# Kernel optimization log

Hardware: AMD Instinct MI355X
Metric: run time of the kernel (lower is better)

Reference implementation:

```python
import jax, jax.numpy as jnp
import numpy as np

B, N, F = 2, 512, 64
LN_EPS = 1e-6

def _ln(x, scale, bias):
    mu = jnp.mean(x, axis=-1, keepdims=True)
    var = jnp.mean(jnp.square(x - mu), axis=-1, keepdims=True)
    return (x - mu) * jax.lax.rsqrt(var + LN_EPS) * scale + bias

def setup_inputs() -> dict:
    key = jax.random.key(0)
    k = jax.random.split(key, 16)
    w = lambda kk, s: jax.random.normal(kk, s, jnp.float32) * 0.02
    return {
        'qs': jax.random.normal(k[0], (B, N, F), jnp.float32),
        'ks': jax.random.normal(k[1], (B, N, F), jnp.float32),
        'vs': jax.random.normal(k[2], (B, N, F), jnp.float32),
        'qs_s': jax.random.normal(k[3], (B, N, 2), jnp.float32),
        'ks_s': jax.random.normal(k[4], (B, N, 2), jnp.float32),
        'qs_t': jax.random.uniform(k[5], (B, N, 1), dtype=jnp.float32),
        'ks_t': jax.random.uniform(k[6], (B, N, 1), dtype=jnp.float32),
        'valid_lens': jax.random.randint(k[7], (B,), 1, N + 1),
        'Wv': w(k[8], (F, 64)), 'bv': jnp.zeros((64,), jnp.float32),
        'Wa1': w(k[9], (2 * F + 5, 256)), 'ba1': jnp.zeros((256,), jnp.float32),
        'Wa2': w(k[10], (256, 256)), 'ba2': jnp.zeros((256,), jnp.float32),
        'Wa3': w(k[11], (256, 1)), 'ba3': jnp.zeros((1,), jnp.float32),
        'Wg1': w(k[12], (64, 256)), 'bg1': jnp.zeros((256,), jnp.float32),
        'Wg2': w(k[13], (256, 64)), 'bg2': jnp.zeros((64,), jnp.float32),
        'ln1_s': jnp.ones((64,), jnp.float32), 'ln1_b': jnp.zeros((64,), jnp.float32),
        'ln2_s': jnp.ones((64,), jnp.float32), 'ln2_b': jnp.zeros((64,), jnp.float32),
    }

def reference(qs, ks, vs, qs_s, ks_s, qs_t, ks_t, valid_lens,
              Wv, bv, Wa1, ba1, Wa2, ba2, Wa3, ba3,
              Wg1, bg1, Wg2, bg2, ln1_s, ln1_b, ln2_s, ln2_b):
    Bb, Q, Ff = qs.shape
    K = ks.shape[1]
    # pairwise broadcast-concat features: (B, Q, K, 2F+5)
    qb = jnp.broadcast_to(qs[:, :, None, :], (Bb, Q, K, Ff))
    kb = jnp.broadcast_to(ks[:, None, :, :], (Bb, Q, K, Ff))
    s_diff = qs_s[:, :, None, :] - ks_s[:, None, :, :]            # (B,Q,K,2)
    s_dist = jnp.linalg.norm(s_diff, axis=-1, keepdims=True)      # (B,Q,K,1)
    t_diff = qs_t[:, :, None, :] - ks_t[:, None, :, :]            # (B,Q,K,1)
    m = jnp.concatenate([qb, kb, s_diff, s_dist, jnp.square(s_dist), t_diff], axis=-1)
    # validity mask over the node axis (Q == K node-set attention)
    v_mask = (jnp.arange(K)[None, :] < valid_lens[:, None])[..., None]  # (B,K,1)
    mask = jnp.logical_and(v_mask, t_diff[..., 0] > 0)                   # (B,Q,K)
    # per-pair MLP attention score
    h = jax.nn.gelu(m @ Wa1 + ba1)
    h = jax.nn.gelu(h @ Wa2 + ba2)
    attn = (h @ Wa3 + ba3)[..., 0]                                       # (B,Q,K)
    attn = jnp.where(mask, attn, 0.0)
    vproj = vs @ Wv + bv                                                 # (B,K,64)
    ctx = _ln(jnp.einsum('bqk,bkd->bqd', attn, vproj), ln1_s, ln1_b)     # (B,Q,64)
    gate = jax.nn.gelu(ctx @ Wg1 + bg1) @ Wg2 + bg2                      # (B,Q,64)
    pooled = jnp.max(jnp.where(v_mask, gate * ctx, -jnp.inf), axis=1)    # (B,64)
    vnode = _ln(pooled, ln2_s, ln2_b)
    return ctx, vnode
```

## Files before the change

kernel.cpp:

```cpp
#include <hip/hip_runtime.h>
#include <math.h>

#define BB 2
#define NN 512
#define FF 64
#define HH 256
#define LN_EPS 1e-6f

typedef __attribute__((ext_vector_type(8))) short short8v;
typedef __attribute__((ext_vector_type(4))) float float4v;

#define LDAH 264

#if __has_builtin(__builtin_amdgcn_exp2f)
#define EXP2F(x) __builtin_amdgcn_exp2f(x)
#else
#define EXP2F(x) exp2f(x)
#endif
#if __has_builtin(__builtin_amdgcn_sqrtf)
#define SQRTF(x) __builtin_amdgcn_sqrtf(x)
#else
#define SQRTF(x) sqrtf(x)
#endif

__device__ __forceinline__ float gelu_tanh(float x) {
    float x2 = x * x;
    float t  = __builtin_fmaf(0.10294340f, x2, 2.30211830f);
    float e  = EXP2F(x * t);
    float r  = __builtin_amdgcn_rcpf(e + 1.0f);
    return __builtin_fmaf(-x, r, x);
}

__device__ __forceinline__ unsigned short f2bf(float f) {
    unsigned u = __float_as_uint(f);
    unsigned r = u + 0x7fffu + ((u >> 16) & 1u);
    return (unsigned short)(r >> 16);
}

__device__ __forceinline__ unsigned enc_f(float f) {
    unsigned b = __float_as_uint(f);
    return (b & 0x80000000u) ? ~b : (b | 0x80000000u);
}
__device__ __forceinline__ float dec_f(unsigned u) {
    return __uint_as_float((u & 0x80000000u) ? (u ^ 0x80000000u) : ~u);
}

__global__ __launch_bounds__(256) void prep_kernel(
    const float* __restrict__ qs, const float* __restrict__ ks,
    const float* __restrict__ vs,
    const float* __restrict__ Wa1, const float* __restrict__ ba1,
    const float* __restrict__ Wv,  const float* __restrict__ bv,
    const float* __restrict__ Wa2,
    const float* __restrict__ qs_t, const float* __restrict__ ks_t,
    const int*   __restrict__ valid_lens,
    const float* __restrict__ ln1_b,
    float* __restrict__ Aq, float* __restrict__ Ak,
    float* __restrict__ vproj, unsigned short* __restrict__ Wa2T,
    int* __restrict__ klist, int* __restrict__ wl,
    unsigned* __restrict__ pooled,
    float* __restrict__ ctx_init) {
    __shared__ int s_cnt[8];
    __shared__ int s_off[9];
    const int bid = blockIdx.x;
    const int t   = threadIdx.x;
    if (bid < 1024) {
        int idx = bid * 256 + t;
        int j  = idx & (HH - 1);
        int bn = idx >> 8;
        const float* qrow = qs + bn * FF;
        const float* krow = ks + bn * FF;
        float aq = ba1[j];
        float ak = 0.0f;
#pragma unroll 8
        for (int f = 0; f < FF; ++f) {
            aq += qrow[f] * Wa1[f * HH + j];
            ak += krow[f] * Wa1[(FF + f) * HH + j];
        }
        Aq[idx] = aq;
        Ak[idx] = ak;
    } else if (bid < 1280) {
        int idx = (bid - 1024) * 256 + t;
        int d  = idx & 63;
        int bn = idx >> 6;
        const float* vrow = vs + bn * FF;
        float a = bv[d];
#pragma unroll 8
        for (int f = 0; f < FF; ++f) a += vrow[f] * Wv[f * 64 + d];
        vproj[idx] = a;
        int q = bn & 511;
        int b = bn >> 9;
        ctx_init[idx] = (q < valid_lens[b]) ? 0.0f : ln1_b[d];
    } else if (bid < 1536) {
        if (bid == 1280 && t < 128) pooled[t] = 0u;
        int idx = (bid - 1280) * 256 + t;
        int n = idx >> 8;
        int i = idx & 255;
        Wa2T[idx] = f2bf(Wa2[i * HH + n]);
    } else {
        const int bq = bid - 1536;
        const int b  = bq >> 9;
        const int q  = bq & 511;
        if (q >= valid_lens[b]) {
            if (t < 8) wl[bq * 8 + t] = bq | (t << 10);
            return;
        }
        const float qt = qs_t[bq];
        const int lane = t & 63;
        const int w    = t >> 6;
        bool validr[2];
        int  posr[2];
#pragma unroll
        for (int r = 0; r < 2; ++r) {
            int k = r * 256 + t;
            float kt = ks_t[b * NN + k];
            bool valid = (qt - kt) > 0.0f;
            unsigned long long bal = __ballot(valid);
            validr[r] = valid;
            posr[r] = (int)__popcll(bal & ((1ull << lane) - 1ull));
            if (lane == 0) s_cnt[r * 4 + w] = (int)__popcll(bal);
        }
        __syncthreads();
        if (t == 0) {
            int acc = 0;
#pragma unroll
            for (int i = 0; i < 8; ++i) { s_off[i] = acc; acc += s_cnt[i]; }
            s_off[8] = acc;
        }
        __syncthreads();
#pragma unroll
        for (int r = 0; r < 2; ++r)
            if (validr[r])
                klist[bq * 512 + s_off[r * 4 + w] + posr[r]] = r * 256 + t;
        const int nk = s_off[8];
        if (t < 8) {
            int nv = nk - (t << 6);
            nv = nv < 0 ? 0 : (nv > 64 ? 64 : nv);
            wl[bq * 8 + t] = bq | (t << 10) | (nv << 13);
        }
    }
}

__global__ __launch_bounds__(256, 3) void attn_ctx_kernel(
    const float* __restrict__ ks_s, const float* __restrict__ qs_s,
    const float* __restrict__ qs_t, const float* __restrict__ ks_t,
    const float* __restrict__ Wa1,
    const unsigned short* __restrict__ Wa2T,
    const float* __restrict__ ba2, const float* __restrict__ Wa3,
    const float* __restrict__ ba3,
    const float* __restrict__ Aq,  const float* __restrict__ Ak,
    const float* __restrict__ vproj,
    const int* __restrict__ klist, const int* __restrict__ wl,
    float* __restrict__ ctx_acc_g) {

    __shared__ unsigned short s_h1[64 * LDAH];
    __shared__ float4 s_feat4[64];
    __shared__ int    s_koe[64];
    __shared__ int    s_kvo[64];
    __shared__ float  s_part[4 * 64];
    __shared__ float  s_attn[64];

    const int e  = wl[blockIdx.x];
    const int nv = (e >> 13) & 127;
    if (nv == 0) return;
    const int bq = e & 1023;
    const int c  = (e >> 10) & 7;
    const int b  = bq >> 9;

    const int t    = threadIdx.x;
    const int lane = t & 63;
    const int w    = t >> 6;
    const int l15  = lane & 15;
    const int quad = lane >> 4;

    const int n0 = w * 64;
    const unsigned short* bbase = Wa2T + (size_t)(n0 + l15) * HH + quad * 8;
    short8v Bcur[4];
#pragma unroll
    for (int nt = 0; nt < 4; ++nt)
        Bcur[nt] = *(const short8v*)(bbase + (size_t)nt * 16 * HH);

    const float qt   = qs_t[bq];
    const float qss0 = qs_s[bq * 2 + 0];
    const float qss1 = qs_s[bq * 2 + 1];
    if (t < 64) {
        int k = klist[bq * 512 + c * 64 + ((t < nv) ? t : 0)];
        int bk = b * NN + k;
        float d0 = qss0 - ks_s[bk * 2 + 0];
        float d1 = qss1 - ks_s[bk * 2 + 1];
        float dist = SQRTF(d0 * d0 + d1 * d1);
        float td = qt - ks_t[bk];
        s_feat4[t] = make_float4(d0, d1, dist, td);
        s_koe[t] = bk * HH;
        s_kvo[t] = bk * 64;
    }
    __syncthreads();

    {
        const int jp = (t & 127) * 2;
        const int kh = (t >> 7) * 32;
        const float2 aqv = *(const float2*)(Aq + bq * HH + jp);
        const float2 w0v = *(const float2*)(Wa1 + 128 * HH + jp);
        const float2 w1v = *(const float2*)(Wa1 + 129 * HH + jp);
        const float2 w2v = *(const float2*)(Wa1 + 130 * HH + jp);
        const float2 w3v = *(const float2*)(Wa1 + 131 * HH + jp);
        const float2 w4v = *(const float2*)(Wa1 + 132 * HH + jp);
        const float* __restrict__ Akj = Ak + jp;
        unsigned* __restrict__ s_h1w = (unsigned*)s_h1;
        const int colw = t & 127;
#pragma unroll
        for (int g = 0; g < 2; ++g) {
            float2 akv[16];
#pragma unroll
            for (int u = 0; u < 16; ++u)
                akv[u] = *(const float2*)(Akj + s_koe[kh + g * 16 + u]);
#pragma unroll
            for (int u = 0; u < 16; ++u) {
                const int kl = kh + g * 16 + u;
                float4 f = s_feat4[kl];
                float fz2 = f.z * f.z;
                float v0 = aqv.x + akv[u].x + w0v.x * f.x + w1v.x * f.y
                         + w2v.x * f.z + w3v.x * fz2 + w4v.x * f.w;
                float v1 = aqv.y + akv[u].y + w0v.y * f.x + w1v.y * f.y
                         + w2v.y * f.z + w3v.y * fz2 + w4v.y * f.w;
                unsigned lo = f2bf(gelu_tanh(v0));
                unsigned hi = f2bf(gelu_tanh(v1));
                s_h1w[kl * (LDAH / 2) + colw] = lo | (hi << 16);
            }
        }
    }
    __syncthreads();

    float4v acc[4][4];
#pragma unroll
    for (int mt = 0; mt < 4; ++mt)
#pragma unroll
        for (int nt = 0; nt < 4; ++nt) acc[mt][nt] = (float4v){0.f, 0.f, 0.f, 0.f};
    const unsigned short* abase = s_h1 + l15 * LDAH + quad * 8;
#pragma unroll
    for (int ksx = 0; ksx < 8; ++ksx) {
        short8v Bnxt[4];
        if (ksx < 7) {
            const int k1 = (ksx + 1) * 32;
#pragma unroll
            for (int nt = 0; nt < 4; ++nt)
                Bnxt[nt] = *(const short8v*)(bbase + (size_t)nt * 16 * HH + k1);
        }
        short8v Af[4];
        const int k0 = ksx * 32;
#pragma unroll
        for (int mt = 0; mt < 4; ++mt)
            Af[mt] = *(const short8v*)(abase + mt * 16 * LDAH + k0);
#pragma unroll
        for (int mt = 0; mt < 4; ++mt)
#pragma unroll
            for (int nt = 0; nt < 4; ++nt)
                acc[mt][nt] = __builtin_amdgcn_mfma_f32_16x16x32_bf16(
                    Af[mt], Bcur[nt], acc[mt][nt], 0, 0, 0);
        if (ksx < 7) {
#pragma unroll
            for (int nt = 0; nt < 4; ++nt) Bcur[nt] = Bnxt[nt];
        }
    }

    {
        float ba2r[4], wa3r[4];
#pragma unroll
        for (int nt = 0; nt < 4; ++nt) {
            int col = n0 + nt * 16 + l15;
            ba2r[nt] = ba2[col];
            wa3r[nt] = Wa3[col];
        }
        float prow[4][4];
#pragma unroll
        for (int mt = 0; mt < 4; ++mt)
#pragma unroll
            for (int r = 0; r < 4; ++r) prow[mt][r] = 0.0f;
#pragma unroll
        for (int mt = 0; mt < 4; ++mt)
#pragma unroll
            for (int nt = 0; nt < 4; ++nt)
#pragma unroll
                for (int r = 0; r < 4; ++r)
                    prow[mt][r] += gelu_tanh(acc[mt][nt][r] + ba2r[nt]) * wa3r[nt];
#pragma unroll
        for (int m = 1; m < 16; m <<= 1)
#pragma unroll
            for (int mt = 0; mt < 4; ++mt)
#pragma unroll
                for (int r = 0; r < 4; ++r)
                    prow[mt][r] += __shfl_xor(prow[mt][r], m);
        if (l15 == 0) {
#pragma unroll
            for (int mt = 0; mt < 4; ++mt)
#pragma unroll
                for (int r = 0; r < 4; ++r)
                    s_part[w * 64 + mt * 16 + quad * 4 + r] = prow[mt][r];
        }
    }
    __syncthreads();

    if (t < 64) {
        float a = 0.0f;
        if (t < nv)
            a = s_part[t] + s_part[64 + t] + s_part[128 + t] + s_part[192 + t] + ba3[0];
        s_attn[t] = a;
    }
    __syncthreads();

    {
        float vv[16];
#pragma unroll
        for (int u = 0; u < 16; ++u)
            vv[u] = vproj[s_kvo[w * 16 + u] + lane];
        float cacc = 0.0f;
#pragma unroll
        for (int u = 0; u < 16; ++u)
            cacc += s_attn[w * 16 + u] * vv[u];
        s_part[w * 64 + lane] = cacc;
    }
    __syncthreads();
    if (t < 64) {
        float v = s_part[t] + s_part[64 + t] + s_part[128 + t] + s_part[192 + t];
        atomicAdd(&ctx_acc_g[bq * 64 + t], v);
    }
}

__global__ __launch_bounds__(256) void gate_kernel(
    float* __restrict__ ctx,
    const float* __restrict__ ln1_s, const float* __restrict__ ln1_b,
    const float* __restrict__ Wg1, const float* __restrict__ bg1,
    const float* __restrict__ Wg2, const float* __restrict__ bg2,
    const int* __restrict__ valid_lens,
    unsigned* __restrict__ pooled) {
    __shared__ float s_ctx[64];
    __shared__ float s_hg[256];
    const int t  = threadIdx.x;
    const int bq = blockIdx.x;
    const int b  = bq >> 9;
    const int q  = bq & 511;
    if (q >= valid_lens[b]) return;
    if (t < 64) {
        float x = ctx[bq * 64 + t];
        float s = x;
#pragma unroll
        for (int m = 1; m < 64; m <<= 1) s += __shfl_xor(s, m);
        float mu = s * (1.0f / 64.0f);
        float dv = x - mu;
        float vv = dv * dv;
#pragma unroll
        for (int m = 1; m < 64; m <<= 1) vv += __shfl_xor(vv, m);
        float rs = rsqrtf(vv * (1.0f / 64.0f) + LN_EPS);
        float y = dv * rs * ln1_s[t] + ln1_b[t];
        ctx[bq * 64 + t] = y;
        s_ctx[t] = y;
    }
    __syncthreads();
    float a = bg1[t];
#pragma unroll 8
    for (int d = 0; d < 64; ++d) a += s_ctx[d] * Wg1[d * 256 + t];
    s_hg[t] = gelu_tanh(a);
    __syncthreads();
    if (t < 64) {
        float g = bg2[t];
#pragma unroll 8
        for (int jj = 0; jj < 256; ++jj) g += s_hg[jj] * Wg2[jj * 64 + t];
        atomicMax(&pooled[b * 64 + t], enc_f(g * s_ctx[t]));
    }
}

__global__ __launch_bounds__(64) void ln2_kernel(
    const unsigned* __restrict__ pooled,
    const float* __restrict__ ln2_s, const float* __restrict__ ln2_b,
    float* __restrict__ vnode_out) {
    const int t = threadIdx.x;
    const int b = blockIdx.x;
    float x = dec_f(pooled[b * 64 + t]);
    float s = x;
#pragma unroll
    for (int mm = 1; mm < 64; mm <<= 1) s += __shfl_xor(s, mm);
    float mu = s * (1.0f / 64.0f);
    float dv = x - mu;
    float vv = dv * dv;
#pragma unroll
    for (int mm = 1; mm < 64; mm <<= 1) vv += __shfl_xor(vv, mm);
    float rs = rsqrtf(vv * (1.0f / 64.0f) + LN_EPS);
    vnode_out[b * 64 + t] = dv * rs * ln2_s[t] + ln2_b[t];
}

extern "C" void kernel_launch(void* const* d_in, const int* in_sizes, int n_in,
                              void* d_out, int out_size, void* d_ws, size_t ws_size,
                              hipStream_t stream) {
    const float* qs   = (const float*)d_in[0];
    const float* ks   = (const float*)d_in[1];
    const float* vs   = (const float*)d_in[2];
    const float* qs_s = (const float*)d_in[3];
    const float* ks_s = (const float*)d_in[4];
    const float* qs_t = (const float*)d_in[5];
    const float* ks_t = (const float*)d_in[6];
    const int*   valid_lens = (const int*)d_in[7];
    const float* Wv   = (const float*)d_in[8];
    const float* bv   = (const float*)d_in[9];
    const float* Wa1  = (const float*)d_in[10];
    const float* ba1  = (const float*)d_in[11];
    const float* Wa2  = (const float*)d_in[12];
    const float* ba2  = (const float*)d_in[13];
    const float* Wa3  = (const float*)d_in[14];
    const float* ba3  = (const float*)d_in[15];
    const float* Wg1  = (const float*)d_in[16];
    const float* bg1  = (const float*)d_in[17];
    const float* Wg2  = (const float*)d_in[18];
    const float* bg2  = (const float*)d_in[19];
    const float* ln1_s = (const float*)d_in[20];
    const float* ln1_b = (const float*)d_in[21];
    const float* ln2_s = (const float*)d_in[22];
    const float* ln2_b = (const float*)d_in[23];

    float* out = (float*)d_out;
    float* ws  = (float*)d_ws;
    float* Aq    = ws;
    float* Ak    = Aq + BB * NN * HH;
    float* vproj = Ak + BB * NN * HH;
    unsigned short* Wa2T = (unsigned short*)(vproj + BB * NN * 64);
    int* klist = (int*)(Wa2T + HH * HH);
    unsigned* pooled = (unsigned*)(klist + BB * NN * 512);
    int* wl = (int*)(pooled + 128);

    prep_kernel<<<2560, 256, 0, stream>>>(qs, ks, vs, Wa1, ba1, Wv, bv, Wa2,
                                          qs_t, ks_t, valid_lens, ln1_b,
                                          Aq, Ak, vproj, Wa2T, klist, wl, pooled, out);
    attn_ctx_kernel<<<8192, 256, 0, stream>>>(ks_s, qs_s, qs_t, ks_t,
                                              Wa1, Wa2T, ba2, Wa3, ba3,
                                              Aq, Ak, vproj,
                                              klist, wl, out);
    gate_kernel<<<BB * NN, 256, 0, stream>>>(out, ln1_s, ln1_b, Wg1, bg1, Wg2, bg2,
                                             valid_lens, pooled);
    ln2_kernel<<<BB, 64, 0, stream>>>(pooled, ln2_s, ln2_b, out + BB * NN * 64);
}
```

Measured before the change: 245.6 us.

## Compact attention work list via atomic counter and precompute pair features in prep

```diff
diff --git a/kernel.cpp b/kernel.cpp
--- a/kernel.cpp
+++ b/kernel.cpp
@@ -51,12 +51,13 @@
     const float* __restrict__ Wa1, const float* __restrict__ ba1,
     const float* __restrict__ Wv,  const float* __restrict__ bv,
     const float* __restrict__ Wa2,
+    const float* __restrict__ qs_s, const float* __restrict__ ks_s,
     const float* __restrict__ qs_t, const float* __restrict__ ks_t,
     const int*   __restrict__ valid_lens,
     const float* __restrict__ ln1_b,
     float* __restrict__ Aq, float* __restrict__ Ak,
     float* __restrict__ vproj, unsigned short* __restrict__ Wa2T,
-    int* __restrict__ klist, int* __restrict__ wl,
+    float4* __restrict__ flist, int* __restrict__ wl_count, int* __restrict__ wl,
     unsigned* __restrict__ pooled,
     float* __restrict__ ctx_init) {
     __shared__ int s_cnt[8];
@@ -100,19 +101,22 @@
         const int bq = bid - 1536;
         const int b  = bq >> 9;
         const int q  = bq & 511;
-        if (q >= valid_lens[b]) {
-            if (t < 8) wl[bq * 8 + t] = bq | (t << 10);
-            return;
-        }
-        const float qt = qs_t[bq];
+        if (q >= valid_lens[b]) return;
+        const float qt   = qs_t[bq];
+        const float qss0 = qs_s[bq * 2 + 0];
+        const float qss1 = qs_s[bq * 2 + 1];
         const int lane = t & 63;
         const int w    = t >> 6;
         bool validr[2];
         int  posr[2];
+        float ktr[2];
+        float2 ksr[2];
 #pragma unroll
         for (int r = 0; r < 2; ++r) {
             int k = r * 256 + t;
             float kt = ks_t[b * NN + k];
+            ksr[r] = *(const float2*)(ks_s + (b * NN + k) * 2);
+            ktr[r] = kt;
             bool valid = (qt - kt) > 0.0f;
             unsigned long long bal = __ballot(valid);
             validr[r] = valid;
@@ -129,27 +133,35 @@
         __syncthreads();
 #pragma unroll
         for (int r = 0; r < 2; ++r)
-            if (validr[r])
-                klist[bq * 512 + s_off[r * 4 + w] + posr[r]] = r * 256 + t;
+            if (validr[r]) {
+                int gpos = s_off[r * 4 + w] + posr[r];
+                float d0 = qss0 - ksr[r].x;
+                float d1 = qss1 - ksr[r].y;
+                float td = qt - ktr[r];
+                flist[bq * 512 + gpos] =
+                    make_float4(d0, d1, td, __int_as_float(r * 256 + t));
+            }
         const int nk = s_off[8];
-        if (t < 8) {
-            int nv = nk - (t << 6);
-            nv = nv < 0 ? 0 : (nv > 64 ? 64 : nv);
-            wl[bq * 8 + t] = bq | (t << 10) | (nv << 13);
+        if (t == 0 && nk > 0) {
+            int nch = (nk + 63) >> 6;
+            int base = atomicAdd(wl_count, nch);
+            for (int c = 0; c < nch; ++c) {
+                int nv = nk - (c << 6);
+                nv = nv > 64 ? 64 : nv;
+                wl[base + c] = bq | (c << 10) | (nv << 13);
+            }
         }
     }
 }
 
 __global__ __launch_bounds__(256, 3) void attn_ctx_kernel(
-    const float* __restrict__ ks_s, const float* __restrict__ qs_s,
-    const float* __restrict__ qs_t, const float* __restrict__ ks_t,
     const float* __restrict__ Wa1,
     const unsigned short* __restrict__ Wa2T,
     const float* __restrict__ ba2, const float* __restrict__ Wa3,
     const float* __restrict__ ba3,
     const float* __restrict__ Aq,  const float* __restrict__ Ak,
     const float* __restrict__ vproj,
-    const int* __restrict__ klist, const int* __restrict__ wl,
+    const float4* __restrict__ flist, const int* __restrict__ wl,
     float* __restrict__ ctx_acc_g) {
 
     __shared__ unsigned short s_h1[64 * LDAH];
@@ -179,31 +191,27 @@
     for (int nt = 0; nt < 4; ++nt)
         Bcur[nt] = *(const short8v*)(bbase + (size_t)nt * 16 * HH);
 
-    const float qt   = qs_t[bq];
-    const float qss0 = qs_s[bq * 2 + 0];
-    const float qss1 = qs_s[bq * 2 + 1];
+    const int jp = (t & 127) * 2;
+    const float2 aqv = *(const float2*)(Aq + bq * HH + jp);
+    const float2 w0v = *(const float2*)(Wa1 + 128 * HH + jp);
+    const float2 w1v = *(const float2*)(Wa1 + 129 * HH + jp);
+    const float2 w2v = *(const float2*)(Wa1 + 130 * HH + jp);
+    const float2 w3v = *(const float2*)(Wa1 + 131 * HH + jp);
+    const float2 w4v = *(const float2*)(Wa1 + 132 * HH + jp);
+
     if (t < 64) {
-        int k = klist[bq * 512 + c * 64 + ((t < nv) ? t : 0)];
+        float4 f = flist[bq * 512 + c * 64 + ((t < nv) ? t : 0)];
+        int k = __float_as_int(f.w);
         int bk = b * NN + k;
-        float d0 = qss0 - ks_s[bk * 2 + 0];
-        float d1 = qss1 - ks_s[bk * 2 + 1];
-        float dist = SQRTF(d0 * d0 + d1 * d1);
-        float td = qt - ks_t[bk];
-        s_feat4[t] = make_float4(d0, d1, dist, td);
+        float dist = SQRTF(f.x * f.x + f.y * f.y);
+        s_feat4[t] = make_float4(f.x, f.y, dist, f.z);
         s_koe[t] = bk * HH;
         s_kvo[t] = bk * 64;
     }
     __syncthreads();
 
     {
-        const int jp = (t & 127) * 2;
         const int kh = (t >> 7) * 32;
-        const float2 aqv = *(const float2*)(Aq + bq * HH + jp);
-        const float2 w0v = *(const float2*)(Wa1 + 128 * HH + jp);
-        const float2 w1v = *(const float2*)(Wa1 + 129 * HH + jp);
-        const float2 w2v = *(const float2*)(Wa1 + 130 * HH + jp);
-        const float2 w3v = *(const float2*)(Wa1 + 131 * HH + jp);
-        const float2 w4v = *(const float2*)(Wa1 + 132 * HH + jp);
         const float* __restrict__ Akj = Ak + jp;
         unsigned* __restrict__ s_h1w = (unsigned*)s_h1;
         const int colw = t & 127;
@@ -236,6 +244,15 @@
 #pragma unroll
         for (int nt = 0; nt < 4; ++nt) acc[mt][nt] = (float4v){0.f, 0.f, 0.f, 0.f};
     const unsigned short* abase = s_h1 + l15 * LDAH + quad * 8;
+
+    float ba2r[4], wa3r[4];
+#pragma unroll
+    for (int nt = 0; nt < 4; ++nt) {
+        int col = n0 + nt * 16 + l15;
+        ba2r[nt] = ba2[col];
+        wa3r[nt] = Wa3[col];
+    }
+
 #pragma unroll
     for (int ksx = 0; ksx < 8; ++ksx) {
         short8v Bnxt[4];
@@ -263,13 +280,6 @@
     }
 
     {
-        float ba2r[4], wa3r[4];
-#pragma unroll
-        for (int nt = 0; nt < 4; ++nt) {
-            int col = n0 + nt * 16 + l15;
-            ba2r[nt] = ba2[col];
-            wa3r[nt] = Wa3[col];
-        }
         float prow[4][4];
 #pragma unroll
         for (int mt = 0; mt < 4; ++mt)
@@ -334,6 +344,7 @@
     unsigned* __restrict__ pooled) {
     __shared__ float s_ctx[64];
     __shared__ float s_hg[256];
+    __shared__ float s_p2[256];
     const int t  = threadIdx.x;
     const int bq = blockIdx.x;
     const int b  = bq >> 9;
@@ -360,10 +371,18 @@
     for (int d = 0; d < 64; ++d) a += s_ctx[d] * Wg1[d * 256 + t];
     s_hg[t] = gelu_tanh(a);
     __syncthreads();
+    {
+        const int d = t & 63, seg = t >> 6;
+        const float* hg = s_hg + seg * 64;
+        const float* w2 = Wg2 + seg * 64 * 64 + d;
+        float g = 0.0f;
+#pragma unroll 8
+        for (int jj = 0; jj < 64; ++jj) g += hg[jj] * w2[jj * 64];
+        s_p2[t] = g;
+    }
+    __syncthreads();
     if (t < 64) {
-        float g = bg2[t];
-#pragma unroll 8
-        for (int jj = 0; jj < 256; ++jj) g += s_hg[jj] * Wg2[jj * 64 + t];
+        float g = bg2[t] + s_p2[t] + s_p2[64 + t] + s_p2[128 + t] + s_p2[192 + t];
         atomicMax(&pooled[b * 64 + t], enc_f(g * s_ctx[t]));
     }
 }
@@ -421,17 +440,19 @@
     float* Ak    = Aq + BB * NN * HH;
     float* vproj = Ak + BB * NN * HH;
     unsigned short* Wa2T = (unsigned short*)(vproj + BB * NN * 64);
-    int* klist = (int*)(Wa2T + HH * HH);
-    unsigned* pooled = (unsigned*)(klist + BB * NN * 512);
-    int* wl = (int*)(pooled + 128);
-
+    int* wl_count = (int*)(Wa2T + HH * HH);
+    int* wl       = wl_count + 64;
+    unsigned* pooled = (unsigned*)(wl + 8192);
+    float4* flist = (float4*)(pooled + 128);
+
+    hipMemsetAsync(wl_count, 0, (64 + 8192) * sizeof(int), stream);
     prep_kernel<<<2560, 256, 0, stream>>>(qs, ks, vs, Wa1, ba1, Wv, bv, Wa2,
-                                          qs_t, ks_t, valid_lens, ln1_b,
-                                          Aq, Ak, vproj, Wa2T, klist, wl, pooled, out);
-    attn_ctx_kernel<<<8192, 256, 0, stream>>>(ks_s, qs_s, qs_t, ks_t,
-                                              Wa1, Wa2T, ba2, Wa3, ba3,
+                                          qs_s, ks_s, qs_t, ks_t, valid_lens, ln1_b,
+                                          Aq, Ak, vproj, Wa2T, flist, wl_count, wl,
+                                          pooled, out);
+    attn_ctx_kernel<<<8192, 256, 0, stream>>>(Wa1, Wa2T, ba2, Wa3, ba3,
                                               Aq, Ak, vproj,
-                                              klist, wl, out);
+                                              flist, wl, out);
     gate_kernel<<<BB * NN, 256, 0, stream>>>(out, ln1_s, ln1_b, Wg1, bg1, Wg2, bg2,
                                              valid_lens, pooled);
     ln2_kernel<<<BB, 64, 0, stream>>>(pooled, ln2_s, ln2_b, out + BB * NN * 64);
```

New measurement: 201.0 us (median of 2 runs). 1.22x faster.
